# Kernel optimization log

Hardware: AMD Instinct MI355X
Metric: run time of the kernel (lower is better)

The kernel has to match this reference:

```python
import jax, jax.numpy as jnp
import numpy as np

N = 100000   # nodes
E = 800000   # edges
F_IN = 96
HID = 96
C = 32       # num_classes
G = 128      # graphs in batch


def _xavier(k, fi, fo):
    s = float(np.sqrt(6.0 / (fi + fo)))
    return jax.random.uniform(k, (fi, fo), jnp.float32, -s, s)


def setup_inputs() -> dict:
    key = jax.random.key(0)
    ks = jax.random.split(key, 8)
    x = jax.random.normal(ks[0], (N, F_IN), jnp.float32)
    edge_index = jax.random.randint(ks[1], (2, E), 0, N, dtype=jnp.int64)
    batch = jnp.sort(jax.random.randint(ks[2], (N,), 0, G, dtype=jnp.int64))
    return {
        "x": x,
        "W0": _xavier(ks[3], F_IN, HID), "b0": jnp.zeros((HID,), jnp.float32),
        "W1": _xavier(ks[4], HID, HID),  "b1": jnp.zeros((HID,), jnp.float32),
        "W2": _xavier(ks[5], HID, C),    "b2": jnp.zeros((C,), jnp.float32),
        "edge_index": edge_index,
        "batch": batch,
    }


def gcn_conv(x, W, b, src, dst):
    """PyG GCNConv: linear transform, add self-loops, sym-normalized scatter-add."""
    n = x.shape[0]
    h = x @ W                                   # [N, F_out]
    loops = jnp.arange(n, dtype=src.dtype)
    s = jnp.concatenate([src, loops])           # [E+N]
    d = jnp.concatenate([dst, loops])
    deg = jax.ops.segment_sum(jnp.ones_like(d, h.dtype), d, num_segments=n)
    dinv = jax.lax.rsqrt(jnp.maximum(deg, 1.0))
    norm = dinv[s] * dinv[d]                    # [E+N]
    out = jax.ops.segment_sum(h[s] * norm[:, None], d, num_segments=n)
    return out + b


def reference(x, W0, b0, W1, b1, W2, b2, edge_index, batch):
    src, dst = edge_index[0], edge_index[1]
    h = gcn_conv(x, W0, b0, src, dst)
    h = h * jax.nn.sigmoid(h)                   # SiLU
    h = gcn_conv(h, W1, b1, src, dst)
    h = h * jax.nn.sigmoid(h)
    h = gcn_conv(h, W2, b2, src, dst)           # [N, C]
    # global max pool + global mean pool per graph
    gmax = jax.ops.segment_max(h, batch, num_segments=G)
    cnt = jax.ops.segment_sum(jnp.ones((h.shape[0],), h.dtype), batch, num_segments=G)
    gmean = jax.ops.segment_sum(h, batch, num_segments=G) / jnp.maximum(cnt, 1.0)[:, None]
    out = jnp.concatenate([gmax, gmean], axis=1)  # [G, 2C]
    return jax.nn.log_softmax(out, axis=1)
```

## Files before the change

kernel.cpp:

```cpp
#include <hip/hip_runtime.h>
#include <hip/hip_fp16.h>
#include <math.h>


typedef _Float16 f16x8 __attribute__((ext_vector_type(8)));
typedef _Float16 f16x4 __attribute__((ext_vector_type(4)));
typedef float f32x4 __attribute__((ext_vector_type(4)));

static __device__ __forceinline__ float silu_f(float v) {
    return v / (1.0f + __expf(-v));
}

static __device__ __forceinline__ int raw_at(const int* __restrict__ raw,
                                             int idx, int f64) {
    return raw[f64 ? 2 * idx : idx];
}

__global__ __launch_bounds__(256) void k_detect(const int* __restrict__ raw,
                                                int* __restrict__ flag) {
    __shared__ int anynz;
    if (threadIdx.x == 0) anynz = 0;
    __syncthreads();
    if (raw[2 * threadIdx.x + 1] != 0) anynz = 1;
    __syncthreads();
    if (threadIdx.x == 0) *flag = (anynz ? 0 : 1);
}

__global__ __launch_bounds__(512) void k_p1hist(const int* __restrict__ eraw,
                                                const int* __restrict__ flag,
                                                int* __restrict__ bcnt,
                                                int E, int nbuk) {
    __shared__ int hs[512];
    const int t = threadIdx.x;
    const int f64 = flag[0];
    hs[t] = 0;
    __syncthreads();
    const int base = blockIdx.x * 8192;
    const int lim = min(base + 8192, E);
    for (int j = base + t; j < lim; j += 512)
        atomicAdd(&hs[raw_at(eraw, E + j, f64) >> 8], 1);
    __syncthreads();
    if (t < nbuk && hs[t]) atomicAdd(&bcnt[t], hs[t]);
}

__global__ __launch_bounds__(512) void k_bscan(const int* __restrict__ bcnt,
                                               int* __restrict__ bstart,
                                               int nbuk, int E) {
    __shared__ int lds[512];
    int t = threadIdx.x;
    int v = (t < nbuk) ? bcnt[t] : 0;
    lds[t] = v;
    __syncthreads();
    for (int off = 1; off < 512; off <<= 1) {
        int y = (t >= off) ? lds[t - off] : 0;
        __syncthreads();
        lds[t] += y;
        __syncthreads();
    }
    if (t < nbuk) bstart[t] = lds[t] - v;
    if (t == 0) bstart[nbuk] = E;
}

__global__ __launch_bounds__(512) void k_p2scatter(const int* __restrict__ eraw,
                                                   const int* __restrict__ flag,
                                                   const int* __restrict__ bstart,
                                                   int* __restrict__ gcursor,
                                                   unsigned* __restrict__ ebuk,
                                                   int E, int nbuk) {
    __shared__ int hs[512], sc[512], lexcl[512], pl[512], gb[512];
    __shared__ unsigned stg[8192];
    __shared__ unsigned short stb[8192];
    const int t = threadIdx.x;
    const int f64 = flag[0];
    const int base = blockIdx.x * 8192;
    const int len = min(8192, E - base);

    hs[t] = 0;
    __syncthreads();
    for (int j = t; j < len; j += 512)
        atomicAdd(&hs[raw_at(eraw, E + base + j, f64) >> 8], 1);
    __syncthreads();

    int cv = (t < nbuk) ? hs[t] : 0;
    sc[t] = cv;
    __syncthreads();
    for (int off = 1; off < 512; off <<= 1) {
        int y = (t >= off) ? sc[t - off] : 0;
        __syncthreads();
        sc[t] += y;
        __syncthreads();
    }
    int ex = sc[t] - cv;
    if (t < nbuk) {
        lexcl[t] = ex;
        pl[t] = ex;
        gb[t] = cv ? atomicAdd(&gcursor[t], cv) : 0;
    }
    __syncthreads();

    for (int j = t; j < len; j += 512) {
        int d = raw_at(eraw, E + base + j, f64);
        int s = raw_at(eraw, base + j, f64);
        int b = d >> 8;
        int slot = atomicAdd(&pl[b], 1);
        stg[slot] = ((unsigned)s << 8) | (unsigned)(d & 255);
        stb[slot] = (unsigned short)b;
    }
    __syncthreads();

    for (int s2 = t; s2 < len; s2 += 512) {
        int b = stb[s2];
        int gpos = bstart[b] + gb[b] + (s2 - lexcl[b]);
        ebuk[gpos] = stg[s2];
    }
}

__global__ __launch_bounds__(256) void k_p3sort(const unsigned* __restrict__ ebuk,
                                                const int* __restrict__ bstart,
                                                int* __restrict__ adj,
                                                int* __restrict__ rowptr,
                                                float* __restrict__ dinv,
                                                int n, int E) {
    const int b = blockIdx.x;
    const int t = threadIdx.x;
    const int s0 = bstart[b], s1 = bstart[b + 1];
    __shared__ int cs[256], pl[256];
    cs[t] = 0;
    __syncthreads();
    for (int j = s0 + t; j < s1; j += 256)
        atomicAdd(&cs[ebuk[j] & 255], 1);
    __syncthreads();
    int cv = cs[t];
    pl[t] = cv;
    __syncthreads();
    for (int off = 1; off < 256; off <<= 1) {
        int y = (t >= off) ? pl[t - off] : 0;
        __syncthreads();
        pl[t] += y;
        __syncthreads();
    }
    int ex = pl[t] - cv;
    __syncthreads();
    pl[t] = ex;
    int node = (b << 8) + t;
    if (node < n) {
        rowptr[node] = s0 + ex;
        dinv[node] = rsqrtf((float)cv + 1.0f);
    }
    if (b == 0 && t == 0) rowptr[n] = E;
    __syncthreads();
    for (int j = s0 + t; j < s1; j += 256) {
        unsigned p = ebuk[j];
        int slot = atomicAdd(&pl[p & 255], 1);
        adj[s0 + slot] = (int)(p >> 8);
    }
}

__global__ __launch_bounds__(256) void k_gstart(const int* __restrict__ braw,
                                                const int* __restrict__ flag,
                                                int* __restrict__ gstart,
                                                int n, int G) {
    int t = threadIdx.x;
    if (t > G) return;
    const int f64 = flag[0];
    int lo = 0, hi = n;
    while (lo < hi) {
        int mid = (lo + hi) >> 1;
        if (raw_at(braw, mid, f64) < t) lo = mid + 1; else hi = mid;
    }
    gstart[t] = lo;
}

__global__ __launch_bounds__(256) void k_wt3(const float* __restrict__ W0,
                                             const float* __restrict__ W1,
                                             const float* __restrict__ W2,
                                             __half* __restrict__ WT) {
    int idx = blockIdx.x * 256 + threadIdx.x;
    if (idx >= 21504) return;
    const float* W;
    int fout, loc;
    if (idx < 9216)       { W = W0; fout = 96; loc = idx; }
    else if (idx < 18432) { W = W1; fout = 96; loc = idx - 9216; }
    else                  { W = W2; fout = 32; loc = idx - 18432; }
    int nn = loc / 96, kk = loc - nn * 96;
    WT[idx] = __float2half(W[kk * fout + nn]);
}

template <int FOUT, bool AHALF>
__global__ __launch_bounds__(256) void k_gemm_mfma(const float* __restrict__ Xf,
                                                   const __half* __restrict__ Xh,
                                                   const __half* __restrict__ WT,
                                                   const float* __restrict__ dinv,
                                                   __half* __restrict__ H, int n) {
    const int l = threadIdx.x & 63;
    const int w = threadIdx.x >> 6;
    const int row0 = blockIdx.x * 64 + w * 16;
    const int lr = l & 15, lg = l >> 4;
    constexpr int NT = FOUT / 16;

    f16x8 bfrag[NT][3];
    #pragma unroll
    for (int t = 0; t < NT; ++t)
        #pragma unroll
        for (int kk = 0; kk < 3; ++kk)
            bfrag[t][kk] = *(const f16x8*)&WT[(t * 16 + lr) * 96 + kk * 32 + lg * 8];

    f32x4 acc[NT];
    #pragma unroll
    for (int t = 0; t < NT; ++t) acc[t] = (f32x4){0.f, 0.f, 0.f, 0.f};

    int arow = row0 + lr;
    int arow_c = arow < n ? arow : n - 1;

    #pragma unroll
    for (int kk = 0; kk < 3; ++kk) {
        f16x8 af;
        if (AHALF) {
            af = *(const f16x8*)(Xh + (size_t)arow_c * 96 + kk * 32 + lg * 8);
        } else {
            const float* xr = Xf + (size_t)arow_c * 96;
            float4 u0 = *(const float4*)&xr[kk * 32 + lg * 8];
            float4 u1 = *(const float4*)&xr[kk * 32 + lg * 8 + 4];
            af[0] = (_Float16)u0.x; af[1] = (_Float16)u0.y;
            af[2] = (_Float16)u0.z; af[3] = (_Float16)u0.w;
            af[4] = (_Float16)u1.x; af[5] = (_Float16)u1.y;
            af[6] = (_Float16)u1.z; af[7] = (_Float16)u1.w;
        }
        #pragma unroll
        for (int t = 0; t < NT; ++t)
            acc[t] = __builtin_amdgcn_mfma_f32_16x16x32_f16(af, bfrag[t][kk], acc[t], 0, 0, 0);
    }

    #pragma unroll
    for (int i = 0; i < 4; ++i) {
        int r = row0 + lg * 4 + i;
        if (r < n) {
            float dv = dinv[r];
            #pragma unroll
            for (int t = 0; t < NT; ++t)
                H[(size_t)r * FOUT + t * 16 + lr] = __float2half(acc[t][i] * dv);
        }
    }
}

template <bool SILU>
__global__ __launch_bounds__(256) void k_agg96(const __half* __restrict__ Hp,
                                               const float* __restrict__ dinv,
                                               const int* __restrict__ rowptr,
                                               const int* __restrict__ adj,
                                               const float* __restrict__ bias,
                                               __half* __restrict__ OUT, int n) {
    const int l = threadIdx.x & 63;
    const int node = blockIdx.x * 4 + (threadIdx.x >> 6);
    if (node >= n) return;
    const int q = l >> 4;
    const int li = l & 15;
    const int oct = li < 12 ? li : li - 12;
    const float dn = dinv[node];
    const int e0 = rowptr[node], e1 = rowptr[node + 1];
    const f16x8* __restrict__ H8 = (const f16x8*)Hp;

    const __half2 one2 = __float2half2_rn(1.f);
    const __half2 zero2 = __float2half2_rn(0.f);

    __half2 hacc[4];
    #pragma unroll
    for (int i = 0; i < 4; ++i) hacc[i] = zero2;

    int vs = 0;
    if (e0 < e1) vs = adj[min(e0 + (l & 7), e1 - 1)];

    {
        f16x8 v = H8[(size_t)node * 12 + oct];
        const __half2* vh = (const __half2*)&v;
        __half2 ws = (q == 0) ? one2 : zero2;
        #pragma unroll
        for (int i = 0; i < 4; ++i) hacc[i] = __hfma2(vh[i], ws, hacc[i]);
    }

    for (int e = e0; e < e1; e += 8) {
        int vs_next = vs;
        if (e + 8 < e1) vs_next = adj[min(e + 8 + (l & 7), e1 - 1)];
        int s0 = __shfl(vs, q, 64);
        int s1 = __shfl(vs, 4 + q, 64);
        __half2 w0 = (e + q < e1) ? one2 : zero2;
        __half2 w1 = (e + 4 + q < e1) ? one2 : zero2;
        f16x8 v0 = H8[(size_t)s0 * 12 + oct];
        f16x8 v1 = H8[(size_t)s1 * 12 + oct];
        const __half2* vh0 = (const __half2*)&v0;
        const __half2* vh1 = (const __half2*)&v1;
        #pragma unroll
        for (int i = 0; i < 4; ++i) hacc[i] = __hfma2(vh0[i], w0, hacc[i]);
        #pragma unroll
        for (int i = 0; i < 4; ++i) hacc[i] = __hfma2(vh1[i], w1, hacc[i]);
        vs = vs_next;
    }

    float acc[8];
    #pragma unroll
    for (int i = 0; i < 4; ++i) {
        float2 f = __half22float2(hacc[i]);
        acc[2 * i] = f.x;
        acc[2 * i + 1] = f.y;
    }
    #pragma unroll
    for (int i = 0; i < 8; ++i) {
        acc[i] += __shfl_xor(acc[i], 16, 64);
        acc[i] += __shfl_xor(acc[i], 32, 64);
    }

    if (l < 12) {
        float4 bv0 = ((const float4*)bias)[2 * l];
        float4 bv1 = ((const float4*)bias)[2 * l + 1];
        float o0 = acc[0] * dn + bv0.x, o1 = acc[1] * dn + bv0.y;
        float o2 = acc[2] * dn + bv0.z, o3 = acc[3] * dn + bv0.w;
        float o4 = acc[4] * dn + bv1.x, o5 = acc[5] * dn + bv1.y;
        float o6 = acc[6] * dn + bv1.z, o7 = acc[7] * dn + bv1.w;
        if (SILU) {
            o0 = silu_f(o0); o1 = silu_f(o1); o2 = silu_f(o2); o3 = silu_f(o3);
            o4 = silu_f(o4); o5 = silu_f(o5); o6 = silu_f(o6); o7 = silu_f(o7);
        }
        f16x8 wv = {(_Float16)o0, (_Float16)o1, (_Float16)o2, (_Float16)o3,
                    (_Float16)o4, (_Float16)o5, (_Float16)o6, (_Float16)o7};
        *(f16x8*)(OUT + (size_t)node * 96 + l * 8) = wv;
    }
}

__global__ __launch_bounds__(256) void k_agg32(const __half* __restrict__ Hp,
                                               const float* __restrict__ dinv,
                                               const int* __restrict__ rowptr,
                                               const int* __restrict__ adj,
                                               const float* __restrict__ bias,
                                               float* __restrict__ OUT, int n) {
    const int l = threadIdx.x & 63;
    const int node = blockIdx.x * 4 + (threadIdx.x >> 6);
    if (node >= n) return;
    const int g = l >> 3;
    const int li = l & 7;
    const float dn = dinv[node];
    const int e0 = rowptr[node], e1 = rowptr[node + 1];
    const f16x4* __restrict__ H4 = (const f16x4*)Hp;

    const __half2 one2 = __float2half2_rn(1.f);
    const __half2 zero2 = __float2half2_rn(0.f);

    __half2 hacc[2] = {zero2, zero2};

    int vs = 0;
    if (e0 < e1) vs = adj[min(e0 + (l & 7), e1 - 1)];

    {
        f16x4 v = H4[(size_t)node * 8 + li];
        const __half2* vh = (const __half2*)&v;
        __half2 ws = (g == 0) ? one2 : zero2;
        #pragma unroll
        for (int i = 0; i < 2; ++i) hacc[i] = __hfma2(vh[i], ws, hacc[i]);
    }

    for (int e = e0; e < e1; e += 8) {
        int vs_next = vs;
        if (e + 8 < e1) vs_next = adj[min(e + 8 + (l & 7), e1 - 1)];
        int src = __shfl(vs, g, 64);
        __half2 w = (e + g < e1) ? one2 : zero2;
        f16x4 v = H4[(size_t)src * 8 + li];
        const __half2* vh = (const __half2*)&v;
        #pragma unroll
        for (int i = 0; i < 2; ++i) hacc[i] = __hfma2(vh[i], w, hacc[i]);
        vs = vs_next;
    }

    float acc[4];
    #pragma unroll
    for (int i = 0; i < 2; ++i) {
        float2 f = __half22float2(hacc[i]);
        acc[2 * i] = f.x;
        acc[2 * i + 1] = f.y;
    }
    #pragma unroll
    for (int i = 0; i < 4; ++i) {
        acc[i] += __shfl_xor(acc[i], 8, 64);
        acc[i] += __shfl_xor(acc[i], 16, 64);
        acc[i] += __shfl_xor(acc[i], 32, 64);
    }

    if (l < 8) {
        float4 bv = ((const float4*)bias)[l];
        float4 o = make_float4(acc[0] * dn + bv.x, acc[1] * dn + bv.y,
                               acc[2] * dn + bv.z, acc[3] * dn + bv.w);
        ((float4*)(OUT + (size_t)node * 32))[l] = o;
    }
}

__global__ __launch_bounds__(256) void k_poollsm(const float* __restrict__ A,
                                                 const int* __restrict__ gstart,
                                                 float* __restrict__ out) {
    int g = blockIdx.x;
    int s0 = gstart[g], s1 = gstart[g + 1];
    int c = threadIdx.x & 31, k = threadIdx.x >> 5;
    float mx = -INFINITY, sm = 0.f;
    for (int nidx = s0 + k; nidx < s1; nidx += 8) {
        float v = A[(size_t)nidx * 32 + c];
        mx = fmaxf(mx, v);
        sm += v;
    }
    __shared__ float smx[8][32], ssm[8][32], pooled[64];
    smx[k][c] = mx;
    ssm[k][c] = sm;
    __syncthreads();
    if (threadIdx.x < 32) {
        float M = smx[0][c], S = ssm[0][c];
        #pragma unroll
        for (int kk = 1; kk < 8; ++kk) {
            M = fmaxf(M, smx[kk][c]);
            S += ssm[kk][c];
        }
        int cnt = s1 - s0;
        pooled[c] = M;
        pooled[32 + c] = S / fmaxf((float)cnt, 1.0f);
    }
    __syncthreads();
    if (threadIdx.x < 64) {
        int l = threadIdx.x;
        float v = pooled[l];
        float m = v;
        #pragma unroll
        for (int o = 32; o > 0; o >>= 1) m = fmaxf(m, __shfl_xor(m, o, 64));
        float e = __expf(v - m);
        float s = e;
        #pragma unroll
        for (int o = 32; o > 0; o >>= 1) s += __shfl_xor(s, o, 64);
        out[g * 64 + l] = v - m - __logf(s);
    }
}

extern "C" void kernel_launch(void* const* d_in, const int* in_sizes, int n_in,
                              void* d_out, int out_size, void* d_ws, size_t ws_size,
                              hipStream_t stream) {
    const float* x  = (const float*)d_in[0];
    const float* W0 = (const float*)d_in[1];
    const float* b0 = (const float*)d_in[2];
    const float* W1 = (const float*)d_in[3];
    const float* b1 = (const float*)d_in[4];
    const float* W2 = (const float*)d_in[5];
    const float* b2 = (const float*)d_in[6];
    const int* ei_raw    = (const int*)d_in[7];
    const int* batch_raw = (const int*)d_in[8];

    const int N = in_sizes[0] / 96;
    const int E = in_sizes[7] / 2;
    const int G = out_size / 64;
    const int NBUK = (N + 255) >> 8;
    float* out = (float*)d_out;

    char* ws = (char*)d_ws;
    size_t off = 0;
    auto alloc = [&](size_t bytes) -> void* {
        void* p = ws + off;
        off += (bytes + 255) & ~(size_t)255;
        return p;
    };
    __half*   Hp96    = (__half*)alloc((size_t)N * 96 * 2);
    __half*   As16    = (__half*)alloc((size_t)N * 96 * 2);
    __half*   Hp32    = (__half*)alloc((size_t)N * 32 * 2);
    float*    D32     = (float*)alloc((size_t)N * 32 * 4);
    float*    dinv    = (float*)alloc((size_t)N * 4);
    int*      rowptr  = (int*)alloc((size_t)(N + 1) * 4);
    int*      adj     = (int*)alloc((size_t)E * 4);
    unsigned* ebuk    = (unsigned*)alloc((size_t)E * 4);
    int*      bcnt    = (int*)alloc(512 * 4);
    int*      bstart  = (int*)alloc(513 * 4);
    int*      gcursor = (int*)alloc(512 * 4);
    int*      flag    = (int*)alloc(256);
    int*      gstart  = (int*)alloc((size_t)(G + 1) * 4);
    __half*   WT      = (__half*)alloc((size_t)21504 * 2);

    (void)hipMemsetAsync(bcnt, 0, 512 * 4, stream);
    (void)hipMemsetAsync(gcursor, 0, 512 * 4, stream);

    k_detect<<<1, 256, 0, stream>>>(ei_raw, flag);

    k_wt3<<<(21504 + 255) / 256, 256, 0, stream>>>(W0, W1, W2, WT);

    const int P2B = (E + 8191) / 8192;
    k_p1hist<<<P2B, 512, 0, stream>>>(ei_raw, flag, bcnt, E, NBUK);
    k_bscan<<<1, 512, 0, stream>>>(bcnt, bstart, NBUK, E);
    k_p2scatter<<<P2B, 512, 0, stream>>>(ei_raw, flag, bstart, gcursor, ebuk, E, NBUK);
    k_p3sort<<<NBUK, 256, 0, stream>>>(ebuk, bstart, adj, rowptr, dinv, N, E);
    k_gstart<<<1, 256, 0, stream>>>(batch_raw, flag, gstart, N, G);

    const int GB = (N + 63) / 64;
    const int AB = (N + 3) / 4;

    k_gemm_mfma<96, false><<<GB, 256, 0, stream>>>(x, (const __half*)nullptr, WT, dinv, Hp96, N);
    k_agg96<true><<<AB, 256, 0, stream>>>(Hp96, dinv, rowptr, adj, b0, As16, N);
    k_gemm_mfma<96, true><<<GB, 256, 0, stream>>>((const float*)nullptr, As16, WT + 9216, dinv, Hp96, N);
    k_agg96<true><<<AB, 256, 0, stream>>>(Hp96, dinv, rowptr, adj, b1, As16, N);
    k_gemm_mfma<32, true><<<GB, 256, 0, stream>>>((const float*)nullptr, As16, WT + 18432, dinv, Hp32, N);
    k_agg32<<<AB, 256, 0, stream>>>(Hp32, dinv, rowptr, adj, b2, D32, N);

    k_poollsm<<<G, 256, 0, stream>>>(D32, gstart, out);
}
```

Before: 248.3 us.

## Map multiple nodes per wavefront in aggregation kernels instead of one

The aggregation kernels now assign 4 nodes (96-wide) or 8 nodes (32-wide) to each 64-lane wavefront. Each lane group walks its own node's neighbour list, bounded by the wave-wide maximum degree. This removes the cross-lane shuffle reduction and makes the output store use all lanes, where before most lanes sat idle at the write. The cost is divergence: a wave iterates to its largest degree, so lanes for low-degree nodes do masked work. Neighbour indices are now loaded 16 or 8 at a time per group.

```diff
diff --git a/kernel.cpp b/kernel.cpp
--- a/kernel.cpp
+++ b/kernel.cpp
@@ -251,67 +251,61 @@
                                                const float* __restrict__ bias,
                                                __half* __restrict__ OUT, int n) {
     const int l = threadIdx.x & 63;
-    const int node = blockIdx.x * 4 + (threadIdx.x >> 6);
-    if (node >= n) return;
-    const int q = l >> 4;
     const int li = l & 15;
     const int oct = li < 12 ? li : li - 12;
-    const float dn = dinv[node];
-    const int e0 = rowptr[node], e1 = rowptr[node + 1];
+    const int node = blockIdx.x * 16 + (threadIdx.x >> 6) * 4 + (l >> 4);
+    const int nodec = node < n ? node : n - 1;
+    const float dn = dinv[nodec];
+    const int e0 = rowptr[nodec];
+    const int deg = rowptr[nodec + 1] - e0;
     const f16x8* __restrict__ H8 = (const f16x8*)Hp;
+
+    int dmax = deg;
+    dmax = max(dmax, __shfl_xor(dmax, 16, 64));
+    dmax = max(dmax, __shfl_xor(dmax, 32, 64));
 
     const __half2 one2 = __float2half2_rn(1.f);
     const __half2 zero2 = __float2half2_rn(0.f);
 
+    int vs = 0;
+    if (deg > 0) vs = adj[min(e0 + li, e0 + deg - 1)];
+
     __half2 hacc[4];
-    #pragma unroll
-    for (int i = 0; i < 4; ++i) hacc[i] = zero2;
-
-    int vs = 0;
-    if (e0 < e1) vs = adj[min(e0 + (l & 7), e1 - 1)];
-
     {
-        f16x8 v = H8[(size_t)node * 12 + oct];
+        f16x8 v = H8[(size_t)nodec * 12 + oct];
         const __half2* vh = (const __half2*)&v;
-        __half2 ws = (q == 0) ? one2 : zero2;
-        #pragma unroll
-        for (int i = 0; i < 4; ++i) hacc[i] = __hfma2(vh[i], ws, hacc[i]);
-    }
-
-    for (int e = e0; e < e1; e += 8) {
-        int vs_next = vs;
-        if (e + 8 < e1) vs_next = adj[min(e + 8 + (l & 7), e1 - 1)];
-        int s0 = __shfl(vs, q, 64);
-        int s1 = __shfl(vs, 4 + q, 64);
-        __half2 w0 = (e + q < e1) ? one2 : zero2;
-        __half2 w1 = (e + 4 + q < e1) ? one2 : zero2;
+        #pragma unroll
+        for (int i = 0; i < 4; ++i) hacc[i] = vh[i];
+    }
+
+    const int qbase = l & 48;
+    for (int j = 0; j < dmax; j += 2) {
+        int s0 = __shfl(vs, qbase | (j & 15), 64);
+        int s1 = __shfl(vs, qbase | ((j + 1) & 15), 64);
+        __half2 w0 = (j < deg) ? one2 : zero2;
+        __half2 w1 = (j + 1 < deg) ? one2 : zero2;
         f16x8 v0 = H8[(size_t)s0 * 12 + oct];
         f16x8 v1 = H8[(size_t)s1 * 12 + oct];
+        if ((j & 15) == 14 && j + 2 < dmax && deg > 0)
+            vs = adj[min(e0 + j + 2 + li, e0 + deg - 1)];
         const __half2* vh0 = (const __half2*)&v0;
         const __half2* vh1 = (const __half2*)&v1;
         #pragma unroll
         for (int i = 0; i < 4; ++i) hacc[i] = __hfma2(vh0[i], w0, hacc[i]);
         #pragma unroll
         for (int i = 0; i < 4; ++i) hacc[i] = __hfma2(vh1[i], w1, hacc[i]);
-        vs = vs_next;
-    }
-
-    float acc[8];
-    #pragma unroll
-    for (int i = 0; i < 4; ++i) {
-        float2 f = __half22float2(hacc[i]);
-        acc[2 * i] = f.x;
-        acc[2 * i + 1] = f.y;
-    }
-    #pragma unroll
-    for (int i = 0; i < 8; ++i) {
-        acc[i] += __shfl_xor(acc[i], 16, 64);
-        acc[i] += __shfl_xor(acc[i], 32, 64);
-    }
-
-    if (l < 12) {
-        float4 bv0 = ((const float4*)bias)[2 * l];
-        float4 bv1 = ((const float4*)bias)[2 * l + 1];
+    }
+
+    if (li < 12 && node < n) {
+        float acc[8];
+        #pragma unroll
+        for (int i = 0; i < 4; ++i) {
+            float2 f = __half22float2(hacc[i]);
+            acc[2 * i] = f.x;
+            acc[2 * i + 1] = f.y;
+        }
+        float4 bv0 = ((const float4*)bias)[2 * li];
+        float4 bv1 = ((const float4*)bias)[2 * li + 1];
         float o0 = acc[0] * dn + bv0.x, o1 = acc[1] * dn + bv0.y;
         float o2 = acc[2] * dn + bv0.z, o3 = acc[3] * dn + bv0.w;
         float o4 = acc[4] * dn + bv1.x, o5 = acc[5] * dn + bv1.y;
@@ -322,7 +316,7 @@
         }
         f16x8 wv = {(_Float16)o0, (_Float16)o1, (_Float16)o2, (_Float16)o3,
                     (_Float16)o4, (_Float16)o5, (_Float16)o6, (_Float16)o7};
-        *(f16x8*)(OUT + (size_t)node * 96 + l * 8) = wv;
+        *(f16x8*)(OUT + (size_t)node * 96 + li * 8) = wv;
     }
 }
 
@@ -333,61 +327,58 @@
                                                const float* __restrict__ bias,
                                                float* __restrict__ OUT, int n) {
     const int l = threadIdx.x & 63;
-    const int node = blockIdx.x * 4 + (threadIdx.x >> 6);
-    if (node >= n) return;
-    const int g = l >> 3;
     const int li = l & 7;
-    const float dn = dinv[node];
-    const int e0 = rowptr[node], e1 = rowptr[node + 1];
+    const int node = blockIdx.x * 32 + (threadIdx.x >> 6) * 8 + (l >> 3);
+    const int nodec = node < n ? node : n - 1;
+    const float dn = dinv[nodec];
+    const int e0 = rowptr[nodec];
+    const int deg = rowptr[nodec + 1] - e0;
     const f16x4* __restrict__ H4 = (const f16x4*)Hp;
+
+    int dmax = deg;
+    dmax = max(dmax, __shfl_xor(dmax, 8, 64));
+    dmax = max(dmax, __shfl_xor(dmax, 16, 64));
+    dmax = max(dmax, __shfl_xor(dmax, 32, 64));
 
     const __half2 one2 = __float2half2_rn(1.f);
     const __half2 zero2 = __float2half2_rn(0.f);
 
-    __half2 hacc[2] = {zero2, zero2};
-
     int vs = 0;
-    if (e0 < e1) vs = adj[min(e0 + (l & 7), e1 - 1)];
-
+    if (deg > 0) vs = adj[min(e0 + li, e0 + deg - 1)];
+
+    __half2 hacc[2];
     {
-        f16x4 v = H4[(size_t)node * 8 + li];
+        f16x4 v = H4[(size_t)nodec * 8 + li];
         const __half2* vh = (const __half2*)&v;
-        __half2 ws = (g == 0) ? one2 : zero2;
-        #pragma unroll
-        for (int i = 0; i < 2; ++i) hacc[i] = __hfma2(vh[i], ws, hacc[i]);
-    }
-
-    for (int e = e0; e < e1; e += 8) {
-        int vs_next = vs;
-        if (e + 8 < e1) vs_next = adj[min(e + 8 + (l & 7), e1 - 1)];
-        int src = __shfl(vs, g, 64);
-        __half2 w = (e + g < e1) ? one2 : zero2;
-        f16x4 v = H4[(size_t)src * 8 + li];
-        const __half2* vh = (const __half2*)&v;
-        #pragma unroll
-        for (int i = 0; i < 2; ++i) hacc[i] = __hfma2(vh[i], w, hacc[i]);
-        vs = vs_next;
-    }
-
-    float acc[4];
-    #pragma unroll
-    for (int i = 0; i < 2; ++i) {
-        float2 f = __half22float2(hacc[i]);
-        acc[2 * i] = f.x;
-        acc[2 * i + 1] = f.y;
-    }
-    #pragma unroll
-    for (int i = 0; i < 4; ++i) {
-        acc[i] += __shfl_xor(acc[i], 8, 64);
-        acc[i] += __shfl_xor(acc[i], 16, 64);
-        acc[i] += __shfl_xor(acc[i], 32, 64);
-    }
-
-    if (l < 8) {
-        float4 bv = ((const float4*)bias)[l];
-        float4 o = make_float4(acc[0] * dn + bv.x, acc[1] * dn + bv.y,
-                               acc[2] * dn + bv.z, acc[3] * dn + bv.w);
-        ((float4*)(OUT + (size_t)node * 32))[l] = o;
+        hacc[0] = vh[0];
+        hacc[1] = vh[1];
+    }
+
+    const int gbase = l & 56;
+    for (int j = 0; j < dmax; j += 2) {
+        int s0 = __shfl(vs, gbase | (j & 7), 64);
+        int s1 = __shfl(vs, gbase | ((j + 1) & 7), 64);
+        __half2 w0 = (j < deg) ? one2 : zero2;
+        __half2 w1 = (j + 1 < deg) ? one2 : zero2;
+        f16x4 v0 = H4[(size_t)s0 * 8 + li];
+        f16x4 v1 = H4[(size_t)s1 * 8 + li];
+        if ((j & 7) == 6 && j + 2 < dmax && deg > 0)
+            vs = adj[min(e0 + j + 2 + li, e0 + deg - 1)];
+        const __half2* vh0 = (const __half2*)&v0;
+        const __half2* vh1 = (const __half2*)&v1;
+        hacc[0] = __hfma2(vh0[0], w0, hacc[0]);
+        hacc[1] = __hfma2(vh0[1], w0, hacc[1]);
+        hacc[0] = __hfma2(vh1[0], w1, hacc[0]);
+        hacc[1] = __hfma2(vh1[1], w1, hacc[1]);
+    }
+
+    if (node < n) {
+        float2 f0 = __half22float2(hacc[0]);
+        float2 f1 = __half22float2(hacc[1]);
+        float4 bv = ((const float4*)bias)[li];
+        float4 o = make_float4(f0.x * dn + bv.x, f0.y * dn + bv.y,
+                               f1.x * dn + bv.z, f1.y * dn + bv.w);
+        ((float4*)(OUT + (size_t)node * 32))[li] = o;
     }
 }
 
@@ -489,14 +480,15 @@
     k_gstart<<<1, 256, 0, stream>>>(batch_raw, flag, gstart, N, G);
 
     const int GB = (N + 63) / 64;
-    const int AB = (N + 3) / 4;
+    const int AB96 = (N + 15) / 16;
+    const int AB32 = (N + 31) / 32;
 
     k_gemm_mfma<96, false><<<GB, 256, 0, stream>>>(x, (const __half*)nullptr, WT, dinv, Hp96, N);
-    k_agg96<true><<<AB, 256, 0, stream>>>(Hp96, dinv, rowptr, adj, b0, As16, N);
+    k_agg96<true><<<AB96, 256, 0, stream>>>(Hp96, dinv, rowptr, adj, b0, As16, N);
     k_gemm_mfma<96, true><<<GB, 256, 0, stream>>>((const float*)nullptr, As16, WT + 9216, dinv, Hp96, N);
-    k_agg96<true><<<AB, 256, 0, stream>>>(Hp96, dinv, rowptr, adj, b1, As16, N);
+    k_agg96<true><<<AB96, 256, 0, stream>>>(Hp96, dinv, rowptr, adj, b1, As16, N);
     k_gemm_mfma<32, true><<<GB, 256, 0, stream>>>((const float*)nullptr, As16, WT + 18432, dinv, Hp32, N);
-    k_agg32<<<AB, 256, 0, stream>>>(Hp32, dinv, rowptr, adj, b2, D32, N);
+    k_agg32<<<AB32, 256, 0, stream>>>(Hp32, dinv, rowptr, adj, b2, D32, N);
 
     k_poollsm<<<G, 256, 0, stream>>>(D32, gstart, out);
 }
```

New measurement: 205.7 us. 1.21x faster.
